# Kernel optimization log

Measured on AMD Instinct MI355X. Metric: run time of the kernel, lower is better.

Reference implementation:

```python
import jax, jax.numpy as jnp
import numpy as np

TEMP = 0.07
MARGIN = 0.5
INFO_NCE_W = 1.0
TRIPLET_W = 0.1
EPS = 1e-6  # torch F.pairwise_distance default eps


def setup_inputs() -> dict:
    key = jax.random.key(0)
    kA, kB = jax.random.split(key)
    B, K, D = 32, 128, 256
    embeddings_A = jax.random.normal(kA, (B, K, D), dtype=jnp.float32)
    embeddings_B = jax.random.normal(kB, (B, K, D), dtype=jnp.float32)
    return {"embeddings_A": embeddings_A, "embeddings_B": embeddings_B}


def reference(embeddings_A, embeddings_B):
    B, K, D = embeddings_A.shape
    N = B * K
    emb_A = embeddings_A.reshape(N, D)
    emb_B = embeddings_B.reshape(N, D)

    # ---- InfoNCE over full N x N similarity matrix ----
    sim = jnp.matmul(emb_A, emb_B.T) / TEMP  # [N, N]
    logp_A2B = jax.nn.log_softmax(sim, axis=1)
    logp_B2A = jax.nn.log_softmax(sim, axis=0)
    diag = jnp.arange(N)
    loss_A2B = -jnp.mean(logp_A2B[diag, diag])
    loss_B2A = -jnp.mean(logp_B2A[diag, diag])
    info_nce_loss = (loss_A2B + loss_B2A) / 2
    pred = jnp.argmax(sim, axis=1)
    acc = jnp.mean((pred == diag).astype(jnp.float32))

    # ---- Hard negative mining (per batch element, batched) ----
    sim_b = jnp.einsum("bkd,bjd->bkj", embeddings_A, embeddings_B)  # [B, K, K]
    eye = jnp.eye(K, dtype=bool)
    sim_masked = jnp.where(eye[None, :, :], -jnp.inf, sim_b)
    hard_idx = jnp.argmax(sim_masked, axis=2)  # [B, K]
    hard_negs = jnp.take_along_axis(embeddings_B, hard_idx[:, :, None], axis=1)  # [B, K, D]

    # ---- Triplet loss ----
    anchor = emb_A
    positive = emb_B
    negative = hard_negs.reshape(N, D)
    pos_dist = jnp.linalg.norm(anchor - positive + EPS, axis=-1)
    neg_dist = jnp.linalg.norm(anchor - negative + EPS, axis=-1)
    triplet_loss = jnp.mean(jax.nn.relu(pos_dist - neg_dist + MARGIN))

    total_loss = INFO_NCE_W * info_nce_loss + TRIPLET_W * triplet_loss
    return total_loss, info_nce_loss, triplet_loss, acc
```

## Files before the change

kernel.cpp:

```cpp
#include <hip/hip_runtime.h>

#define NR 4096
#define DDIM 256
#define INVT (1.0f/0.07f)

typedef short short8 __attribute__((ext_vector_type(8)));
typedef float floatx4 __attribute__((ext_vector_type(4)));
typedef unsigned short u16;
typedef unsigned int u32;

__device__ __forceinline__ u16 f2bf(float f){
  u32 u = __float_as_uint(f);
  return (u16)((u + 0x7fffu + ((u >> 16) & 1u)) >> 16);
}

__device__ __forceinline__ void async_copy16(const u16* g, u16* l){
  __builtin_amdgcn_global_load_lds(
      (const __attribute__((address_space(1))) void*)g,
      (__attribute__((address_space(3))) void*)l, 16, 0, 0);
}

__device__ __forceinline__ int aload_i(const int* p){
  return __hip_atomic_load(p, __ATOMIC_RELAXED, __HIP_MEMORY_SCOPE_AGENT);
}
__device__ __forceinline__ float aload_f(const float* p){
  return __hip_atomic_load(p, __ATOMIC_RELAXED, __HIP_MEMORY_SCOPE_AGENT);
}

__global__ void k_convert(const float* __restrict__ A, const float* __restrict__ B,
                          u16* __restrict__ Abf, u16* __restrict__ Bbf,
                          int* __restrict__ zero_region){
  if (blockIdx.x == 0) zero_region[threadIdx.x] = 0;
  int t = blockIdx.x * 256 + threadIdx.x;
  const int Q = (NR * DDIM) / 4;
  const float4* src = (t < Q) ? (const float4*)A : (const float4*)B;
  u16* dst = (t < Q) ? Abf : Bbf;
  int idx = (t < Q) ? t : t - Q;
  float4 v = src[idx];
  ushort4 o;
  o.x = f2bf(v.x); o.y = f2bf(v.y); o.z = f2bf(v.z); o.w = f2bf(v.w);
  ((ushort4*)dst)[idx] = o;
}

__global__ __launch_bounds__(256) void k_gemm_stats(
    const u16* __restrict__ Abf, const u16* __restrict__ Bbf,
    float* __restrict__ rp_max, float* __restrict__ rp_sum,
    float* __restrict__ cp_max, float* __restrict__ cp_sum,
    float* __restrict__ sim_diag, int* __restrict__ hard_idx)
{
  __shared__ u16 ldsA[128*64];
  __shared__ u16 ldsB[128*64];

  const int bid = blockIdx.x;
  const int xc = bid & 7, qv = bid >> 3;
  const int rblk = (qv >> 5)*8 + xc;
  const int cblk = qv & 31;

  const int t = threadIdx.x;
  const int w = t >> 6, lane = t & 63;
  const int wr = w >> 1, wc = w & 1;
  const int g = lane >> 4, li = lane & 15;

  floatx4 acc[4][4];
  const floatx4 zz = {0.f,0.f,0.f,0.f};
#pragma unroll
  for (int a = 0; a < 4; ++a)
#pragma unroll
    for (int b = 0; b < 4; ++b) acc[a][b] = zz;

  const int lrow = lane >> 3;
  const int olog = (lane & 7) ^ lrow;
  const u16* baseA = Abf + rblk*128*DDIM;
  const u16* baseB = Bbf + cblk*128*DDIM;

  for (int ki = 0; ki < 4; ++ki){
    if (ki) __syncthreads();
    const int k0 = ki*64;
#pragma unroll
    for (int j = 0; j < 4; ++j){
      int c = w*4 + j;
      int r = c*8 + lrow;
      async_copy16(baseA + r*DDIM + k0 + olog*8, ldsA + c*512);
      async_copy16(baseB + r*DDIM + k0 + olog*8, ldsB + c*512);
    }
    __syncthreads();
#pragma unroll
    for (int ks = 0; ks < 2; ++ks){
      short8 af[4], bfr[4];
      const int o = ks*4 + g;
      const int p8 = (o ^ (li & 7)) * 8;
#pragma unroll
      for (int rf = 0; rf < 4; ++rf)
        af[rf] = *(const short8*)(ldsA + (wr*64 + rf*16 + li)*64 + p8);
#pragma unroll
      for (int cf = 0; cf < 4; ++cf)
        bfr[cf] = *(const short8*)(ldsB + (wc*64 + cf*16 + li)*64 + p8);
#pragma unroll
      for (int rf = 0; rf < 4; ++rf)
#pragma unroll
        for (int cf = 0; cf < 4; ++cf)
          acc[rf][cf] = __builtin_amdgcn_mfma_f32_16x16x32_bf16(af[rf], bfr[cf], acc[rf][cf], 0, 0, 0);
    }
  }
  __syncthreads();

#pragma unroll
  for (int rf = 0; rf < 4; ++rf)
#pragma unroll
    for (int cf = 0; cf < 4; ++cf) acc[rf][cf] *= INVT;

  const bool isdiag = (rblk == cblk);

  float* rm = (float*)ldsA;
  float* rs = rm + 256;
  float* cm = rs + 256;
  float* cs = cm + 256;
  float* hm = cs + 256;
  int*   hj = (int*)(hm + 256);

  {
    float cmv[4], csv[4];
#pragma unroll
    for (int cf = 0; cf < 4; ++cf){
      float m = -3.0e38f;
#pragma unroll
      for (int rf = 0; rf < 4; ++rf)
#pragma unroll
        for (int q = 0; q < 4; ++q) m = fmaxf(m, acc[rf][cf][q]);
      cmv[cf] = m;
    }
#pragma unroll
    for (int s = 16; s < 64; s <<= 1)
#pragma unroll
      for (int cf = 0; cf < 4; ++cf) cmv[cf] = fmaxf(cmv[cf], __shfl_xor(cmv[cf], s));
#pragma unroll
    for (int cf = 0; cf < 4; ++cf){
      float sum = 0.f;
#pragma unroll
      for (int rf = 0; rf < 4; ++rf)
#pragma unroll
        for (int q = 0; q < 4; ++q) sum += __expf(acc[rf][cf][q] - cmv[cf]);
      csv[cf] = sum;
    }
#pragma unroll
    for (int s = 16; s < 64; s <<= 1)
#pragma unroll
      for (int cf = 0; cf < 4; ++cf) csv[cf] += __shfl_xor(csv[cf], s);
    if (g == 0){
#pragma unroll
      for (int cf = 0; cf < 4; ++cf){
        int c = wc*64 + cf*16 + li;
        cm[c*2 + wr] = cmv[cf]; cs[c*2 + wr] = csv[cf];
      }
    }
  }

  if (isdiag){
    if (wr == wc){
#pragma unroll
      for (int rf = 0; rf < 4; ++rf)
#pragma unroll
        for (int q = 0; q < 4; ++q)
          if (g*4 + q == li) sim_diag[rblk*128 + wr*64 + rf*16 + li] = acc[rf][rf][q];
    }
    float hmv[16]; int hjv[16];
#pragma unroll
    for (int rf = 0; rf < 4; ++rf)
#pragma unroll
      for (int q = 0; q < 4; ++q){
        int rowb = wr*64 + rf*16 + g*4 + q;
        float m = -3.0e38f; int bj = 0;
#pragma unroll
        for (int cf = 0; cf < 4; ++cf){
          int colb = wc*64 + cf*16 + li;
          float v = (colb == rowb) ? -3.4e38f : acc[rf][cf][q];
          if (v > m){ m = v; bj = colb; }
        }
        hmv[rf*4+q] = m; hjv[rf*4+q] = bj;
      }
#pragma unroll
    for (int s = 1; s < 16; s <<= 1)
#pragma unroll
      for (int i = 0; i < 16; ++i){
        float om = __shfl_xor(hmv[i], s);
        int   oj = __shfl_xor(hjv[i], s);
        if (om > hmv[i] || (om == hmv[i] && oj < hjv[i])){ hmv[i] = om; hjv[i] = oj; }
      }
    if (li == 0){
#pragma unroll
      for (int rf = 0; rf < 4; ++rf)
#pragma unroll
        for (int q = 0; q < 4; ++q){
          int rowb = wr*64 + rf*16 + g*4 + q;
          hm[rowb*2 + wc] = hmv[rf*4+q]; hj[rowb*2 + wc] = hjv[rf*4+q];
        }
    }
  }

  {
    float m16[16];
#pragma unroll
    for (int rf = 0; rf < 4; ++rf)
#pragma unroll
      for (int q = 0; q < 4; ++q){
        float m = -3.0e38f;
#pragma unroll
        for (int cf = 0; cf < 4; ++cf) m = fmaxf(m, acc[rf][cf][q]);
        m16[rf*4+q] = m;
      }
#pragma unroll
    for (int s = 1; s < 16; s <<= 1)
#pragma unroll
      for (int i = 0; i < 16; ++i) m16[i] = fmaxf(m16[i], __shfl_xor(m16[i], s));
    float s16v[16];
#pragma unroll
    for (int rf = 0; rf < 4; ++rf)
#pragma unroll
      for (int q = 0; q < 4; ++q){
        float sum = 0.f;
#pragma unroll
        for (int cf = 0; cf < 4; ++cf) sum += __expf(acc[rf][cf][q] - m16[rf*4+q]);
        s16v[rf*4+q] = sum;
      }
#pragma unroll
    for (int s = 1; s < 16; s <<= 1)
#pragma unroll
      for (int i = 0; i < 16; ++i) s16v[i] += __shfl_xor(s16v[i], s);
    if (li == 0){
#pragma unroll
      for (int rf = 0; rf < 4; ++rf)
#pragma unroll
        for (int q = 0; q < 4; ++q){
          int r = wr*64 + rf*16 + g*4 + q;
          rm[r*2 + wc] = m16[rf*4+q]; rs[r*2 + wc] = s16v[rf*4+q];
        }
    }
  }

  __syncthreads();

  if (t < 128){
    float m1 = rm[t*2], m2 = rm[t*2+1], s1 = rs[t*2], s2 = rs[t*2+1];
    float M = fmaxf(m1, m2);
    float S = s1*__expf(m1 - M) + s2*__expf(m2 - M);
    rp_max[cblk*NR + rblk*128 + t] = M;
    rp_sum[cblk*NR + rblk*128 + t] = S;
    m1 = cm[t*2]; m2 = cm[t*2+1]; s1 = cs[t*2]; s2 = cs[t*2+1];
    M = fmaxf(m1, m2);
    S = s1*__expf(m1 - M) + s2*__expf(m2 - M);
    cp_max[rblk*NR + cblk*128 + t] = M;
    cp_sum[rblk*NR + cblk*128 + t] = S;
    if (isdiag){
      float h1 = hm[t*2], h2 = hm[t*2+1]; int j1 = hj[t*2], j2 = hj[t*2+1];
      hard_idx[rblk*128 + t] = (h2 > h1 || (h2 == h1 && j2 < j1)) ? j2 : j1;
    }
  }
}

__global__ __launch_bounds__(256) void k_merge_triplet(
    const float* __restrict__ rp_max, const float* __restrict__ rp_sum,
    const float* __restrict__ cp_max, const float* __restrict__ cp_sum,
    const float* __restrict__ sim_diag, const float* __restrict__ A,
    const float* __restrict__ B, const int* __restrict__ hard_idx,
    float* __restrict__ accums, int* __restrict__ flag_cnt, int* __restrict__ flag_list)
{
  __shared__ float sred[8];
  const int b = blockIdx.x;
  const int t = threadIdx.x, w = t >> 6, lane = t & 63;
  if (b < 16){
    int i = b*256 + t;
    float mv[32], sv[32];
#pragma unroll
    for (int s = 0; s < 32; ++s) mv[s] = rp_max[s*NR + i];
    float M = mv[0];
#pragma unroll
    for (int s = 1; s < 32; ++s) M = fmaxf(M, mv[s]);
#pragma unroll
    for (int s = 0; s < 32; ++s) sv[s] = rp_sum[s*NR + i];
    float S = 0.f;
#pragma unroll
    for (int s = 0; s < 32; ++s) S += sv[s]*__expf(mv[s] - M);
    float d = sim_diag[i];
    float a2b = d - (M + __logf(S));
    bool flag = (M - d) < 20.0f;
#pragma unroll
    for (int s = 0; s < 32; ++s) mv[s] = cp_max[s*NR + i];
    float Mc = mv[0];
#pragma unroll
    for (int s = 1; s < 32; ++s) Mc = fmaxf(Mc, mv[s]);
#pragma unroll
    for (int s = 0; s < 32; ++s) sv[s] = cp_sum[s*NR + i];
    float Sc = 0.f;
#pragma unroll
    for (int s = 0; s < 32; ++s) Sc += sv[s]*__expf(mv[s] - Mc);
    float b2a = d - (Mc + __logf(Sc));
    if (flag){
      int p = atomicAdd(flag_cnt, 1);
      if (p < 64) flag_list[p] = i;
    }
    for (int s = 1; s < 64; s <<= 1){ a2b += __shfl_xor(a2b, s); b2a += __shfl_xor(b2a, s); }
    if (lane == 0){ sred[w] = a2b; sred[4 + w] = b2a; }
    __syncthreads();
    if (t == 0){
      atomicAdd(&accums[0], sred[0]+sred[1]+sred[2]+sred[3]);
      atomicAdd(&accums[1], sred[4]+sred[5]+sred[6]+sred[7]);
    }
  } else {
    int i = (b - 16)*4 + w;
    const float4* a4 = (const float4*)(A + i*DDIM);
    const float4* b4 = (const float4*)(B + i*DDIM);
    int nr = (i & ~127) + hard_idx[i];
    const float4* n4 = (const float4*)(B + nr*DDIM);
    float4 a = a4[lane], bb = b4[lane], nv = n4[lane];
    float px = a.x-bb.x+1e-6f, py = a.y-bb.y+1e-6f, pz = a.z-bb.z+1e-6f, pw = a.w-bb.w+1e-6f;
    float qx = a.x-nv.x+1e-6f, qy = a.y-nv.y+1e-6f, qz = a.z-nv.z+1e-6f, qw = a.w-nv.w+1e-6f;
    float pd = px*px + py*py + pz*pz + pw*pw;
    float nd = qx*qx + qy*qy + qz*qz + qw*qw;
    for (int s = 1; s < 64; s <<= 1){ pd += __shfl_xor(pd, s); nd += __shfl_xor(nd, s); }
    if (lane == 0) sred[w] = fmaxf(0.f, sqrtf(pd) - sqrtf(nd) + 0.5f);
    __syncthreads();
    if (t == 0) atomicAdd(&accums[2], sred[0]+sred[1]+sred[2]+sred[3]);
  }
}

__global__ __launch_bounds__(256) void k_fixup_out(
    const float* __restrict__ A, const float* __restrict__ B,
    const int* __restrict__ flag_cnt, const int* __restrict__ flag_list,
    int* __restrict__ viol, int* __restrict__ done_cnt,
    const float* __restrict__ accums, float* __restrict__ out)
{
  __shared__ int spos;
  const int b = blockIdx.x;
  const int t = threadIdx.x;
  int n = *flag_cnt; if (n > 64) n = 64;
  for (int f = 0; f < n; ++f){
    int i = flag_list[f];
    const float4* a4 = (const float4*)(A + i*DDIM);
    const float4* bi = (const float4*)(B + i*DDIM);
    float dd = 0.f;
    for (int k = 0; k < 64; ++k){
      float4 a = a4[k], bv = bi[k];
      dd += a.x*bv.x + a.y*bv.y + a.z*bv.z + a.w*bv.w;
    }
    if (t < 128){
      int j = b*128 + t;
      if (j != i){
        const float4* bj = (const float4*)(B + j*DDIM);
        float s = 0.f;
        for (int k = 0; k < 64; ++k){
          float4 a = a4[k], bv = bj[k];
          s += a.x*bv.x + a.y*bv.y + a.z*bv.z + a.w*bv.w;
        }
        if (s >= dd) atomicAdd(&viol[f], 1);
      }
    }
  }
  __threadfence();
  __syncthreads();
  if (t == 0) spos = atomicAdd(done_cnt, 1);
  __syncthreads();
  if (spos == 31 && t == 0){
    int good = 0;
    for (int f = 0; f < n; ++f) if (aload_i(&viol[f]) == 0) ++good;
    float lossA = -aload_f(&accums[0]) / 4096.f;
    float lossB = -aload_f(&accums[1]) / 4096.f;
    float info = 0.5f*(lossA + lossB);
    float trip = aload_f(&accums[2]) / 4096.f;
    out[0] = info + 0.1f*trip;
    out[1] = info;
    out[2] = trip;
    out[3] = (float)good / 4096.f;
  }
}

extern "C" void kernel_launch(void* const* d_in, const int* in_sizes, int n_in,
                              void* d_out, int out_size, void* d_ws, size_t ws_size,
                              hipStream_t stream)
{
  const float* A = (const float*)d_in[0];
  const float* B = (const float*)d_in[1];
  float* out = (float*)d_out;
  char* ws = (char*)d_ws;

  float* accums     = (float*)ws;
  int*   flag_cnt   = (int*)(ws + 64);
  int*   flag_list  = (int*)(ws + 128);
  int*   viol       = (int*)(ws + 448);
  int*   done_cnt   = (int*)(ws + 768);
  u16*   Abf        = (u16*)(ws + 1024);
  u16*   Bbf        = Abf + NR*DDIM;
  float* rp_max     = (float*)(ws + 1024 + 2*NR*DDIM*sizeof(u16));
  float* rp_sum     = rp_max + 32*NR;
  float* cp_max     = rp_sum + 32*NR;
  float* cp_sum     = cp_max + 32*NR;
  float* sim_diag   = cp_sum + 32*NR;
  int*   hard_idx   = (int*)(sim_diag + NR);

  k_convert<<<2048, 256, 0, stream>>>(A, B, Abf, Bbf, (int*)ws);
  k_gemm_stats<<<1024, 256, 0, stream>>>(Abf, Bbf, rp_max, rp_sum,
                                         cp_max, cp_sum, sim_diag, hard_idx);
  k_merge_triplet<<<1040, 256, 0, stream>>>(rp_max, rp_sum, cp_max, cp_sum, sim_diag,
                                            A, B, hard_idx, accums, flag_cnt, flag_list);
  k_fixup_out<<<32, 256, 0, stream>>>(A, B, flag_cnt, flag_list, viol, done_cnt,
                                      accums, out);
}
```

Baseline: 112.5 us.

## Halve GEMM row tile to 64 and write column partials directly

Shrinks the similarity GEMM tile from 128x128 to 64x128, doubling the grid to 2048 blocks. Each of the 4 waves now owns a 32-column strip, and column softmax partials go straight to global memory, which removes the cross-wave LDS merge for columns. Row and hard-negative partials are merged across 4 waves instead of 2. The merge kernel now reduces 64 column partials per index, so it reads twice as much partial data. B tiles are also loaded twice as often, trading lower reuse for more parallelism and occupancy.

```diff
diff --git a/kernel.cpp b/kernel.cpp
--- a/kernel.cpp
+++ b/kernel.cpp
@@ -48,7 +48,7 @@
     float* __restrict__ cp_max, float* __restrict__ cp_sum,
     float* __restrict__ sim_diag, int* __restrict__ hard_idx)
 {
-  __shared__ u16 ldsA[128*64];
+  __shared__ u16 ldsA[64*64];
   __shared__ u16 ldsB[128*64];
 
   const int bid = blockIdx.x;
@@ -58,47 +58,51 @@
 
   const int t = threadIdx.x;
   const int w = t >> 6, lane = t & 63;
-  const int wr = w >> 1, wc = w & 1;
   const int g = lane >> 4, li = lane & 15;
 
-  floatx4 acc[4][4];
+  floatx4 acc[4][2];
   const floatx4 zz = {0.f,0.f,0.f,0.f};
 #pragma unroll
   for (int a = 0; a < 4; ++a)
 #pragma unroll
-    for (int b = 0; b < 4; ++b) acc[a][b] = zz;
+    for (int b = 0; b < 2; ++b) acc[a][b] = zz;
 
   const int lrow = lane >> 3;
   const int olog = (lane & 7) ^ lrow;
-  const u16* baseA = Abf + rblk*128*DDIM;
+  const u16* baseA = Abf + rblk*64*DDIM;
   const u16* baseB = Bbf + cblk*128*DDIM;
 
   for (int ki = 0; ki < 4; ++ki){
     if (ki) __syncthreads();
     const int k0 = ki*64;
 #pragma unroll
+    for (int j = 0; j < 2; ++j){
+      int c = w*2 + j;
+      int r = c*8 + lrow;
+      async_copy16(baseA + r*DDIM + k0 + olog*8, ldsA + c*512);
+    }
+#pragma unroll
     for (int j = 0; j < 4; ++j){
       int c = w*4 + j;
       int r = c*8 + lrow;
-      async_copy16(baseA + r*DDIM + k0 + olog*8, ldsA + c*512);
       async_copy16(baseB + r*DDIM + k0 + olog*8, ldsB + c*512);
     }
     __syncthreads();
 #pragma unroll
     for (int ks = 0; ks < 2; ++ks){
-      short8 af[4], bfr[4];
+      short8 af[4], bfr[2];
       const int o = ks*4 + g;
       const int p8 = (o ^ (li & 7)) * 8;
 #pragma unroll
       for (int rf = 0; rf < 4; ++rf)
-        af[rf] = *(const short8*)(ldsA + (wr*64 + rf*16 + li)*64 + p8);
-#pragma unroll
-      for (int cf = 0; cf < 4; ++cf)
-        bfr[cf] = *(const short8*)(ldsB + (wc*64 + cf*16 + li)*64 + p8);
-#pragma unroll
-      for (int rf = 0; rf < 4; ++rf)
-#pragma unroll
-        for (int cf = 0; cf < 4; ++cf)
+        af[rf] = *(const short8*)(ldsA + (rf*16 + li)*64 + p8);
+#pragma unroll
+      for (int cf = 0; cf < 2; ++cf)
+        bfr[cf] = *(const short8*)(ldsB + (w*32 + cf*16 + li)*64 + p8);
+#pragma unroll
+      for (int rf = 0; rf < 4; ++rf)
+#pragma unroll
+        for (int cf = 0; cf < 2; ++cf)
           acc[rf][cf] = __builtin_amdgcn_mfma_f32_16x16x32_bf16(af[rf], bfr[cf], acc[rf][cf], 0, 0, 0);
     }
   }
@@ -107,21 +111,20 @@
 #pragma unroll
   for (int rf = 0; rf < 4; ++rf)
 #pragma unroll
-    for (int cf = 0; cf < 4; ++cf) acc[rf][cf] *= INVT;
-
-  const bool isdiag = (rblk == cblk);
+    for (int cf = 0; cf < 2; ++cf) acc[rf][cf] *= INVT;
+
+  const bool isdiag = ((rblk >> 1) == cblk);
+  const int doff = (rblk & 1)*64;
 
   float* rm = (float*)ldsA;
   float* rs = rm + 256;
-  float* cm = rs + 256;
-  float* cs = cm + 256;
-  float* hm = cs + 256;
+  float* hm = rs + 256;
   int*   hj = (int*)(hm + 256);
 
   {
-    float cmv[4], csv[4];
-#pragma unroll
-    for (int cf = 0; cf < 4; ++cf){
+    float cmv[2], csv[2];
+#pragma unroll
+    for (int cf = 0; cf < 2; ++cf){
       float m = -3.0e38f;
 #pragma unroll
       for (int rf = 0; rf < 4; ++rf)
@@ -132,9 +135,9 @@
 #pragma unroll
     for (int s = 16; s < 64; s <<= 1)
 #pragma unroll
-      for (int cf = 0; cf < 4; ++cf) cmv[cf] = fmaxf(cmv[cf], __shfl_xor(cmv[cf], s));
-#pragma unroll
-    for (int cf = 0; cf < 4; ++cf){
+      for (int cf = 0; cf < 2; ++cf) cmv[cf] = fmaxf(cmv[cf], __shfl_xor(cmv[cf], s));
+#pragma unroll
+    for (int cf = 0; cf < 2; ++cf){
       float sum = 0.f;
 #pragma unroll
       for (int rf = 0; rf < 4; ++rf)
@@ -145,36 +148,75 @@
 #pragma unroll
     for (int s = 16; s < 64; s <<= 1)
 #pragma unroll
-      for (int cf = 0; cf < 4; ++cf) csv[cf] += __shfl_xor(csv[cf], s);
+      for (int cf = 0; cf < 2; ++cf) csv[cf] += __shfl_xor(csv[cf], s);
     if (g == 0){
 #pragma unroll
-      for (int cf = 0; cf < 4; ++cf){
-        int c = wc*64 + cf*16 + li;
-        cm[c*2 + wr] = cmv[cf]; cs[c*2 + wr] = csv[cf];
-      }
+      for (int cf = 0; cf < 2; ++cf){
+        int c = cblk*128 + w*32 + cf*16 + li;
+        cp_max[rblk*NR + c] = cmv[cf];
+        cp_sum[rblk*NR + c] = csv[cf];
+      }
+    }
+  }
+
+  {
+    float m16[16];
+#pragma unroll
+    for (int rf = 0; rf < 4; ++rf)
+#pragma unroll
+      for (int q = 0; q < 4; ++q){
+        float m = fmaxf(acc[rf][0][q], acc[rf][1][q]);
+        m16[rf*4+q] = m;
+      }
+#pragma unroll
+    for (int s = 1; s < 16; s <<= 1)
+#pragma unroll
+      for (int i = 0; i < 16; ++i) m16[i] = fmaxf(m16[i], __shfl_xor(m16[i], s));
+    float s16v[16];
+#pragma unroll
+    for (int rf = 0; rf < 4; ++rf)
+#pragma unroll
+      for (int q = 0; q < 4; ++q){
+        s16v[rf*4+q] = __expf(acc[rf][0][q] - m16[rf*4+q]) + __expf(acc[rf][1][q] - m16[rf*4+q]);
+      }
+#pragma unroll
+    for (int s = 1; s < 16; s <<= 1)
+#pragma unroll
+      for (int i = 0; i < 16; ++i) s16v[i] += __shfl_xor(s16v[i], s);
+    if (li == 0){
+#pragma unroll
+      for (int rf = 0; rf < 4; ++rf)
+#pragma unroll
+        for (int q = 0; q < 4; ++q){
+          int r = rf*16 + g*4 + q;
+          rm[r*4 + w] = m16[rf*4+q]; rs[r*4 + w] = s16v[rf*4+q];
+        }
     }
   }
 
   if (isdiag){
-    if (wr == wc){
-#pragma unroll
-      for (int rf = 0; rf < 4; ++rf)
-#pragma unroll
-        for (int q = 0; q < 4; ++q)
-          if (g*4 + q == li) sim_diag[rblk*128 + wr*64 + rf*16 + li] = acc[rf][rf][q];
-    }
+#pragma unroll
+    for (int rf = 0; rf < 4; ++rf)
+#pragma unroll
+      for (int cf = 0; cf < 2; ++cf)
+#pragma unroll
+        for (int q = 0; q < 4; ++q){
+          int rloc = rf*16 + g*4 + q;
+          int cloc = w*32 + cf*16 + li;
+          if (cloc == doff + rloc) sim_diag[rblk*64 + rloc] = acc[rf][cf][q];
+        }
     float hmv[16]; int hjv[16];
 #pragma unroll
     for (int rf = 0; rf < 4; ++rf)
 #pragma unroll
       for (int q = 0; q < 4; ++q){
-        int rowb = wr*64 + rf*16 + g*4 + q;
+        int rloc = rf*16 + g*4 + q;
         float m = -3.0e38f; int bj = 0;
 #pragma unroll
-        for (int cf = 0; cf < 4; ++cf){
-          int colb = wc*64 + cf*16 + li;
-          float v = (colb == rowb) ? -3.4e38f : acc[rf][cf][q];
-          if (v > m){ m = v; bj = colb; }
+        for (int cf = 0; cf < 2; ++cf){
+          int cloc = w*32 + cf*16 + li;
+          float v = (cloc == doff + rloc) ? -3.4e38f : acc[rf][cf][q];
+          if (v > m){ m = v; bj = cloc; }
         }
         hmv[rf*4+q] = m; hjv[rf*4+q] = bj;
       }
@@ -191,68 +233,29 @@
       for (int rf = 0; rf < 4; ++rf)
 #pragma unroll
         for (int q = 0; q < 4; ++q){
-          int rowb = wr*64 + rf*16 + g*4 + q;
-          hm[rowb*2 + wc] = hmv[rf*4+q]; hj[rowb*2 + wc] = hjv[rf*4+q];
+          int r = rf*16 + g*4 + q;
+          hm[r*4 + w] = hmv[rf*4+q]; hj[r*4 + w] = hjv[rf*4+q];
         }
     }
   }
 
-  {
-    float m16[16];
-#pragma unroll
-    for (int rf = 0; rf < 4; ++rf)
-#pragma unroll
-      for (int q = 0; q < 4; ++q){
-        float m = -3.0e38f;
-#pragma unroll
-        for (int cf = 0; cf < 4; ++cf) m = fmaxf(m, acc[rf][cf][q]);
-        m16[rf*4+q] = m;
-      }
-#pragma unroll
-    for (int s = 1; s < 16; s <<= 1)
-#pragma unroll
-      for (int i = 0; i < 16; ++i) m16[i] = fmaxf(m16[i], __shfl_xor(m16[i], s));
-    float s16v[16];
-#pragma unroll
-    for (int rf = 0; rf < 4; ++rf)
-#pragma unroll
-      for (int q = 0; q < 4; ++q){
-        float sum = 0.f;
-#pragma unroll
-        for (int cf = 0; cf < 4; ++cf) sum += __expf(acc[rf][cf][q] - m16[rf*4+q]);
-        s16v[rf*4+q] = sum;
-      }
-#pragma unroll
-    for (int s = 1; s < 16; s <<= 1)
-#pragma unroll
-      for (int i = 0; i < 16; ++i) s16v[i] += __shfl_xor(s16v[i], s);
-    if (li == 0){
-#pragma unroll
-      for (int rf = 0; rf < 4; ++rf)
-#pragma unroll
-        for (int q = 0; q < 4; ++q){
-          int r = wr*64 + rf*16 + g*4 + q;
-          rm[r*2 + wc] = m16[rf*4+q]; rs[r*2 + wc] = s16v[rf*4+q];
-        }
-    }
-  }
-
   __syncthreads();
 
-  if (t < 128){
-    float m1 = rm[t*2], m2 = rm[t*2+1], s1 = rs[t*2], s2 = rs[t*2+1];
-    float M = fmaxf(m1, m2);
-    float S = s1*__expf(m1 - M) + s2*__expf(m2 - M);
-    rp_max[cblk*NR + rblk*128 + t] = M;
-    rp_sum[cblk*NR + rblk*128 + t] = S;
-    m1 = cm[t*2]; m2 = cm[t*2+1]; s1 = cs[t*2]; s2 = cs[t*2+1];
-    M = fmaxf(m1, m2);
-    S = s1*__expf(m1 - M) + s2*__expf(m2 - M);
-    cp_max[rblk*NR + cblk*128 + t] = M;
-    cp_sum[rblk*NR + cblk*128 + t] = S;
+  if (t < 64){
+    float m0 = rm[t*4], m1 = rm[t*4+1], m2 = rm[t*4+2], m3 = rm[t*4+3];
+    float M = fmaxf(fmaxf(m0, m1), fmaxf(m2, m3));
+    float S = rs[t*4]*__expf(m0 - M) + rs[t*4+1]*__expf(m1 - M)
+            + rs[t*4+2]*__expf(m2 - M) + rs[t*4+3]*__expf(m3 - M);
+    rp_max[cblk*NR + rblk*64 + t] = M;
+    rp_sum[cblk*NR + rblk*64 + t] = S;
     if (isdiag){
-      float h1 = hm[t*2], h2 = hm[t*2+1]; int j1 = hj[t*2], j2 = hj[t*2+1];
-      hard_idx[rblk*128 + t] = (h2 > h1 || (h2 == h1 && j2 < j1)) ? j2 : j1;
+      float hM = hm[t*4]; int hJ = hj[t*4];
+#pragma unroll
+      for (int k = 1; k < 4; ++k){
+        float om = hm[t*4+k]; int oj = hj[t*4+k];
+        if (om > hM || (om == hM && oj < hJ)){ hM = om; hJ = oj; }
+      }
+      hard_idx[rblk*64 + t] = hJ;
     }
   }
 }
@@ -283,16 +286,21 @@
     float d = sim_diag[i];
     float a2b = d - (M + __logf(S));
     bool flag = (M - d) < 20.0f;
-#pragma unroll
-    for (int s = 0; s < 32; ++s) mv[s] = cp_max[s*NR + i];
-    float Mc = mv[0];
-#pragma unroll
-    for (int s = 1; s < 32; ++s) Mc = fmaxf(Mc, mv[s]);
-#pragma unroll
-    for (int s = 0; s < 32; ++s) sv[s] = cp_sum[s*NR + i];
+    float cmv[64];
+#pragma unroll
+    for (int s = 0; s < 64; ++s) cmv[s] = cp_max[s*NR + i];
+    float Mc = cmv[0];
+#pragma unroll
+    for (int s = 1; s < 64; ++s) Mc = fmaxf(Mc, cmv[s]);
     float Sc = 0.f;
 #pragma unroll
-    for (int s = 0; s < 32; ++s) Sc += sv[s]*__expf(mv[s] - Mc);
+    for (int c = 0; c < 8; ++c){
+      float cs[8];
+#pragma unroll
+      for (int j = 0; j < 8; ++j) cs[j] = cp_sum[(c*8+j)*NR + i];
+#pragma unroll
+      for (int j = 0; j < 8; ++j) Sc += cs[j]*__expf(cmv[c*8+j] - Mc);
+    }
     float b2a = d - (Mc + __logf(Sc));
     if (flag){
       int p = atomicAdd(flag_cnt, 1);
@@ -392,12 +400,12 @@
   float* rp_max     = (float*)(ws + 1024 + 2*NR*DDIM*sizeof(u16));
   float* rp_sum     = rp_max + 32*NR;
   float* cp_max     = rp_sum + 32*NR;
-  float* cp_sum     = cp_max + 32*NR;
-  float* sim_diag   = cp_sum + 32*NR;
+  float* cp_sum     = cp_max + 64*NR;
+  float* sim_diag   = cp_sum + 64*NR;
   int*   hard_idx   = (int*)(sim_diag + NR);
 
   k_convert<<<2048, 256, 0, stream>>>(A, B, Abf, Bbf, (int*)ws);
-  k_gemm_stats<<<1024, 256, 0, stream>>>(Abf, Bbf, rp_max, rp_sum,
+  k_gemm_stats<<<2048, 256, 0, stream>>>(Abf, Bbf, rp_max, rp_sum,
                                          cp_max, cp_sum, sim_diag, hard_idx);
   k_merge_triplet<<<1040, 256, 0, stream>>>(rp_max, rp_sum, cp_max, cp_sum, sim_diag,
                                             A, B, hard_idx, accums, flag_cnt, flag_list);
```

New measurement: 116.3 us. 3.4% more time.
